# Optimization experiments

Measured on AMD Instinct MI355X. Metric: run time of the kernel, lower is better.

## Reference

```python
import jax, jax.numpy as jnp
import numpy as np

BS, N_LINKS, MAX_LEN = 8192, 512, 32
D_LINK, D_PATH, D_READ, N_OUT = 32, 128, 256, 3
BN_EPS = 1e-5


def setup_inputs() -> dict:
    key = jax.random.key(0)
    ks = jax.random.split(key, 16)
    capa = jax.random.uniform(ks[0], (BS, N_LINKS), jnp.float32, 0.5, 1.0) * 100.0
    avail = jax.random.uniform(ks[1], (BS, N_LINKS), jnp.float32) * capa
    loss = jax.random.uniform(ks[2], (BS, N_LINKS), jnp.float32) * 0.05
    demand = jax.random.uniform(ks[3], (BS,), jnp.float32) * 10.0
    path = jax.random.randint(ks[4], (BS, MAX_LEN), 0, N_LINKS)
    hop_num = jax.random.randint(ks[5], (BS,), 1, MAX_LEN + 1)
    s = 0.1
    inp = {
        "demand": demand,
        "link_avail_capacity": avail,
        "link_capacity": capa,
        "link_loss": loss,
        "path": path,
        "hop_num": hop_num,
        # GRU params (PyTorch layout: [3H, D] gates ordered r,z,n)
        "gru_w_ih": jax.random.normal(ks[6], (3 * D_PATH, D_LINK), jnp.float32) * s,
        "gru_w_hh": jax.random.normal(ks[7], (3 * D_PATH, D_PATH), jnp.float32) * s,
        "gru_b_ih": jax.random.normal(ks[8], (3 * D_PATH,), jnp.float32) * s,
        "gru_b_hh": jax.random.normal(ks[9], (3 * D_PATH,), jnp.float32) * s,
        "bn_gamma": jnp.ones((D_PATH,), jnp.float32),
        "bn_beta": jnp.zeros((D_PATH,), jnp.float32),
        # stacked readout heads [N_OUT, ...]
        "rW1": jax.random.normal(ks[10], (N_OUT, D_PATH, D_READ), jnp.float32) * s,
        "rb1": jnp.zeros((N_OUT, D_READ), jnp.float32),
        "rW2": jax.random.normal(ks[11], (N_OUT, D_READ, D_READ), jnp.float32) * s,
        "rb2": jnp.zeros((N_OUT, D_READ), jnp.float32),
        "rW3": jax.random.normal(ks[12], (N_OUT, D_READ, 1), jnp.float32) * s,
        "rb3": jnp.zeros((N_OUT, 1), jnp.float32),
    }
    return inp


def _gru_scan(x_bt, h0, w_ih, w_hh, b_ih, b_hh):
    # x_bt: [B, T, D]; h0: [B, H] -> outputs [B, T, H]
    H = h0.shape[-1]
    def step(h, x_t):
        gi = x_t @ w_ih.T + b_ih          # [B, 3H]
        gh = h @ w_hh.T + b_hh            # [B, 3H]
        i_r, i_z, i_n = gi[:, :H], gi[:, H:2*H], gi[:, 2*H:]
        h_r, h_z, h_n = gh[:, :H], gh[:, H:2*H], gh[:, 2*H:]
        r = jax.nn.sigmoid(i_r + h_r)
        z = jax.nn.sigmoid(i_z + h_z)
        n = jnp.tanh(i_n + r * h_n)
        h_new = (1.0 - z) * n + z * h
        return h_new, h_new
    _, outs = jax.lax.scan(step, h0, jnp.swapaxes(x_bt, 0, 1))
    return jnp.swapaxes(outs, 0, 1)


def reference(demand, link_avail_capacity, link_capacity, link_loss, path, hop_num,
              gru_w_ih, gru_w_hh, gru_b_ih, gru_b_hh, bn_gamma, bn_beta,
              rW1, rb1, rW2, rb2, rW3, rb3):
    bs, n_links = link_capacity.shape
    max_len = path.shape[1]
    max_capa = jax.lax.stop_gradient(jnp.max(link_capacity))
    # link_state: [B, n_links, D_LINK]; first D_LINK-4 channels are zeros
    feats = jnp.stack([
        link_avail_capacity / max_capa,
        link_capacity / max_capa,
        link_avail_capacity / link_capacity,
        link_loss,
    ], axis=-1)
    link_state = jnp.concatenate(
        [jnp.zeros((bs, n_links, D_LINK - 4), feats.dtype), feats], axis=-1)
    link_state = jax.lax.stop_gradient(link_state)  # original detaches
    # initial hidden: zeros except last channel = demand/max_capa
    h0 = jnp.concatenate(
        [jnp.zeros((bs, D_PATH - 1), feats.dtype), (demand / max_capa)[:, None]], axis=-1)
    # fused gather of link states along each path, masked past hop_num
    gathered = jnp.take_along_axis(link_state, path[:, :, None], axis=1)  # [B, T, D]
    mask = (jnp.arange(max_len)[None, :] < hop_num[:, None])[:, :, None]
    link_inputs = gathered * mask.astype(gathered.dtype)
    outputs = _gru_scan(link_inputs, h0, gru_w_ih, gru_w_hh, gru_b_ih, gru_b_hh)
    # extract hidden state at last hop of each path
    idx = (hop_num - 1)[:, None, None]
    flow = jnp.take_along_axis(outputs, idx, axis=1)[:, 0, :]  # [B, H]
    # BatchNorm1d (training mode: batch statistics, biased variance)
    mean = jnp.mean(flow, axis=0)
    var = jnp.mean((flow - mean) ** 2, axis=0)
    flow = (flow - mean) * jax.lax.rsqrt(var + BN_EPS) * bn_gamma + bn_beta
    # readout heads: Linear -> SELU -> Linear -> SELU -> Linear
    h1 = jax.nn.selu(jnp.einsum('bh,uhr->ubr', flow, rW1) + rb1[:, None, :])
    h2 = jax.nn.selu(jnp.einsum('ubr,urs->ubs', h1, rW2) + rb2[:, None, :])
    y = jnp.einsum('ubs,uso->ubo', h2, rW3) + rb3[:, None, :]  # [U, B, 1]
    return jnp.transpose(y[:, :, 0], (1, 0))  # [B, U]
```

## Files before the change

kernel.cpp:

```cpp
#include <hip/hip_runtime.h>


#define BS 8192
#define NL 512
#define ML 32
#define DP 128
#define DR 256
#define NJOB 512
#define ST 172

#define OFF_SUM    64
#define OFF_SSQ    192
#define OFF_CUR    576
#define OFF_PERM   640
#define OFF_WHH16  (OFF_PERM + BS)
#define OFF_W1     (OFF_WHH16 + 24576)
#define OFF_W2     (OFF_W1 + 49152)
#define OFF_FEATS  (OFF_W2 + 98304)
#define OFF_FLOW   (OFF_FEATS + BS*ML*4)

#define MAX_BLOCKS   256
#define WPREP_BLOCKS 336
#define SORT_BID     (MAX_BLOCKS + WPREP_BLOCKS)
#define PREP_GRID    (SORT_BID + 1)

#define KS (-1.44269504088896340736f)
#define KT ( 2.88539008177792681472f)

typedef _Float16 f16x8 __attribute__((ext_vector_type(8)));
typedef _Float16 f16x4 __attribute__((ext_vector_type(4)));
typedef float    f32x4 __attribute__((ext_vector_type(4)));

__device__ __forceinline__ float sig2_(float x){
  return __builtin_amdgcn_rcpf(1.0f + exp2f(x));
}
__device__ __forceinline__ float tanh2_(float v){
  return fmaf(-2.0f, __builtin_amdgcn_rcpf(1.0f + exp2f(v)), 1.0f);
}
__device__ __forceinline__ float seluf_(float x){
  const float sc = 1.0507009873554805f, al = 1.6732632423543772f;
  return x > 0.0f ? sc*x : sc*al*(__expf(x)-1.0f);
}

__global__ void prep_all(const int* __restrict__ path, const int* __restrict__ hop,
                         const float* __restrict__ avail, const float* __restrict__ capa,
                         const float* __restrict__ loss, const float* __restrict__ whh,
                         const float* __restrict__ rW1, const float* __restrict__ rW2,
                         float* ws){
  const int bid = blockIdx.x;
  const int tid = threadIdx.x;

  if (bid < MAX_BLOCKS){
    const float4* c4 = (const float4*)capa;
    const int n4 = BS*NL/4;
    float m = 0.0f;
    for (int i = bid*256 + tid; i < n4; i += MAX_BLOCKS*256){
      float4 v = c4[i];
      m = fmaxf(m, fmaxf(fmaxf(v.x, v.y), fmaxf(v.z, v.w)));
    }
    #pragma unroll
    for (int o = 32; o > 0; o >>= 1) m = fmaxf(m, __shfl_down(m, o, 64));
    if ((tid & 63) == 0) atomicMax((int*)ws, __float_as_int(m));
  } else if (bid < SORT_BID){
    _Float16* whh16 = (_Float16*)(ws + OFF_WHH16);
    _Float16* w1    = (_Float16*)(ws + OFF_W1);
    _Float16* w2    = (_Float16*)(ws + OFF_W2);
    int base = (bid - MAX_BLOCKS)*1024 + tid*4;
    if (base < 49152){
      const float s = (base < 32768) ? KS : KT;
      const float4 v = *(const float4*)(whh + base);
      f16x4 o = { (_Float16)(v.x*s), (_Float16)(v.y*s),
                  (_Float16)(v.z*s), (_Float16)(v.w*s) };
      *(f16x4*)(whh16 + base) = o;
    } else if (base < 147456){
      int j = base - 49152; int u = j >> 15; int rem = j & 32767; int n = rem >> 7; int k = rem & 127;
      const float* src = rW1 + u*32768 + k*256 + n;
      f16x4 o = { (_Float16)src[0], (_Float16)src[256], (_Float16)src[512], (_Float16)src[768] };
      *(f16x4*)(w1 + j) = o;
    } else {
      int j = base - 147456; int u = j >> 16; int rem = j & 65535; int n = rem >> 8; int k = rem & 255;
      const float* src = rW2 + u*65536 + k*256 + n;
      f16x4 o = { (_Float16)src[0], (_Float16)src[256], (_Float16)src[512], (_Float16)src[768] };
      *(f16x4*)(w2 + j) = o;
    }
  } else {
    __shared__ int hist[32], start[32];
    for (int i = 64 + tid; i < 640; i += 256) ws[i] = 0.0f;
    if (tid < 32) hist[tid] = 0;
    __syncthreads();
    for (int b = tid; b < BS; b += 256) atomicAdd(&hist[32 - hop[b]], 1);
    __syncthreads();
    if (tid == 0){ int acc = 0; for (int i = 0; i < 32; ++i){ start[i] = acc; acc += hist[i]; } }
    __syncthreads();
    int* perm = (int*)ws + OFF_PERM;
    for (int b = tid; b < BS; b += 256){
      int pos = atomicAdd(&start[32 - hop[b]], 1);
      perm[pos] = b;
    }
  }
}

__launch_bounds__(512, 4)
__global__ void kgru(const float* __restrict__ demand, const int* __restrict__ hop,
                     const float* __restrict__ wih, const float* __restrict__ bih,
                     const float* __restrict__ bhh,
                     const float* __restrict__ avail, const float* __restrict__ capa,
                     const float* __restrict__ loss, const int* __restrict__ path,
                     float* __restrict__ ws, float* __restrict__ flow){
  __shared__ _Float16 hA[2][16*ST];
  const int tid  = threadIdx.x;
  const int w    = tid >> 6;
  const int lane = tid & 63;
  const int lm   = lane & 15;
  const int qd   = lane >> 4;
  const int ch   = w*16 + lm;
  const float inv_maxc = 1.0f / ws[0];
  const int* perm = (const int*)ws + OFF_PERM;
  const _Float16* whh16 = (const _Float16*)(ws + OFF_WHH16);

  const int bid = blockIdx.x;
  const int q = (bid < 256) ? bid : 767 - bid;

  for (int idx = tid; idx < 1024; idx += 512){
    const int buf = idx >> 9;
    const int rem = idx & 511;
    const int m   = rem >> 5;
    const int c   = 128 + (rem & 31);
    hA[buf][m*ST + c] = (_Float16)0.f;
  }

  f16x8 bfr[5], bfz[5], bfnh[4], bfni;
  #pragma unroll
  for (int kc = 0; kc < 4; ++kc){
    bfr[kc]  = *(const f16x8*)(whh16 + (      ch)*128 + kc*32 + qd*8);
    bfz[kc]  = *(const f16x8*)(whh16 + (128 + ch)*128 + kc*32 + qd*8);
    bfnh[kc] = *(const f16x8*)(whh16 + (256 + ch)*128 + kc*32 + qd*8);
  }
  bfr[4] = (f16x8)0; bfz[4] = (f16x8)0; bfni = (f16x8)0;
  if (qd == 0){
    #pragma unroll
    for (int j = 0; j < 4; ++j){
      float s = (j < 2) ? inv_maxc : 1.0f;
      bfr[4][j] = (_Float16)(wih[(      ch)*32 + 28 + j] * s * KS);
      bfz[4][j] = (_Float16)(wih[(128 + ch)*32 + 28 + j] * s * KS);
      bfni[j]   = (_Float16)(wih[(256 + ch)*32 + 28 + j] * s * KT);
    }
  }
  const float bR  = (bih[ch]     + bhh[ch]    ) * KS;
  const float bZ  = (bih[128+ch] + bhh[128+ch]) * KS;
  const float bNI = bih[256+ch] * KT;
  const float bNH = bhh[256+ch] * KT;

  int it[4], hp[4];
  #pragma unroll
  for (int r = 0; r < 4; ++r){
    it[r] = perm[q*16 + qd*4 + r];
    hp[r] = hop[it[r]];
  }
  int tmax = max(max(hp[0],hp[1]), max(hp[2],hp[3]));
  tmax = max(tmax, __shfl_xor(tmax, 16, 64));
  tmax = max(tmax, __shfl_xor(tmax, 32, 64));

  const int  fw_i = w*2 + (lane >> 2);
  const int  fw_c = lane & 3;
  const bool fw   = (lane < 8);
  const float* pX   = avail;
  const int*   pPath = path;
  if (fw){
    const int fw_b = perm[q*16 + fw_i];
    pX = ((fw_c == 0) ? avail : (fw_c == 3) ? loss : capa) + fw_b*NL;
    pPath = path + fw_b*ML;
  }

  __syncthreads();

  float hprev[4];
  #pragma unroll
  for (int r = 0; r < 4; ++r){
    float h0 = (ch == 127) ? demand[it[r]] * inv_maxc : 0.0f;
    hprev[r] = h0;
    hA[0][(qd*4 + r)*ST + ch] = (_Float16)h0;
  }
  float rawB = 0.f;
  int   lA   = 0;
  if (fw){
    int l0 = pPath[0];
    float r0 = pX[l0];
    float a  = __shfl(r0, lane & ~3, 64);
    float cc = __shfl(r0, (lane & ~3) | 1, 64);
    float v0 = (fw_c == 2) ? (a / cc) : r0;
    hA[0][fw_i*ST + 128 + fw_c] = (_Float16)v0;
    rawB = pX[pPath[1]];
    lA   = pPath[2];
  }
  __syncthreads();

  for (int t = 0; t < tmax; ++t){
    const int cur = t & 1, nxt = cur ^ 1;

    float rawN = 0.f; int lN = 0;
    if (fw){
      rawN = pX[lA];
      int t3 = t + 3; t3 = (t3 < ML) ? t3 : (ML - 1);
      lN = pPath[t3];
      float a  = __shfl(rawB, lane & ~3, 64);
      float cc = __shfl(rawB, (lane & ~3) | 1, 64);
      float v  = (fw_c == 2) ? (a / cc) : rawB;
      hA[nxt][fw_i*ST + 128 + fw_c] = (_Float16)v;
    }

    f32x4 accr  = {bR, bR, bR, bR};
    f32x4 accz  = {bZ, bZ, bZ, bZ};
    f32x4 accnh = {bNH, bNH, bNH, bNH};
    f32x4 accni = {bNI, bNI, bNI, bNI};
    #pragma unroll
    for (int kc = 0; kc < 5; ++kc){
      f16x8 a = *(const f16x8*)(&hA[cur][lm*ST + kc*32 + qd*8]);
      accr = __builtin_amdgcn_mfma_f32_16x16x32_f16(a, bfr[kc], accr, 0, 0, 0);
      accz = __builtin_amdgcn_mfma_f32_16x16x32_f16(a, bfz[kc], accz, 0, 0, 0);
      if (kc < 4)
        accnh = __builtin_amdgcn_mfma_f32_16x16x32_f16(a, bfnh[kc], accnh, 0, 0, 0);
      else
        accni = __builtin_amdgcn_mfma_f32_16x16x32_f16(a, bfni, accni, 0, 0, 0);
    }

    #pragma unroll
    for (int r = 0; r < 4; ++r){
      float rr = sig2_(accr[r]);
      float zz = sig2_(accz[r]);
      float nn = tanh2_(fmaf(rr, accnh[r], accni[r]));
      float hn = fmaf(zz, hprev[r] - nn, nn);
      if (t < hp[r]) hprev[r] = hn;
      hA[nxt][(qd*4 + r)*ST + ch] = (_Float16)hprev[r];
    }
    rawB = rawN; lA = lN;
    __syncthreads();
  }

  float ssum = 0.f, ssq = 0.f;
  #pragma unroll
  for (int r = 0; r < 4; ++r){
    float v = hprev[r];
    flow[it[r]*DP + ch] = v;
    ssum += v;
    ssq  = fmaf(v, v, ssq);
  }
  ssum += __shfl_xor(ssum, 16, 64);  ssum += __shfl_xor(ssum, 32, 64);
  ssq  += __shfl_xor(ssq,  16, 64);  ssq  += __shfl_xor(ssq,  32, 64);
  if (qd == 0){
    atomicAdd(&ws[OFF_SUM + ch], ssum);
    atomicAdd(&ws[OFF_SSQ + ch], ssq);
  }
}

__launch_bounds__(256, 4)
__global__ void kmlp(const float* __restrict__ flow, const float* __restrict__ ws,
                     const float* __restrict__ gamma, const float* __restrict__ beta,
                     const float* __restrict__ rb1, const float* __restrict__ rb2,
                     const float* __restrict__ rW3, const float* __restrict__ rb3,
                     float* __restrict__ out){
  __shared__ _Float16 x_lds[32*136];
  __shared__ _Float16 h1_lds[32*264];
  __shared__ float aa[DP], bb[DP];
  __shared__ float y_part[4][32];
  const int tid  = threadIdx.x;
  const int w    = tid >> 6;
  const int lane = tid & 63;
  const int lm   = lane & 15;
  const int qd   = lane >> 4;
  const int b0   = blockIdx.x * 32;
  const int u    = blockIdx.y;
  const _Float16* w1 = (const _Float16*)(ws + OFF_W1) + u*(DR*DP);
  const _Float16* w2 = (const _Float16*)(ws + OFF_W2) + u*(DR*DR);

  if (tid < DP){
    float m = ws[OFF_SUM + tid] * (1.0f/BS);
    float q = ws[OFF_SSQ + tid] * (1.0f/BS);
    float rstd = rsqrtf(q - m*m + 1e-5f);
    float a = rstd * gamma[tid];
    aa[tid] = a;
    bb[tid] = fmaf(-m, a, beta[tid]);
  }
  __syncthreads();

  for (int idx = tid; idx < 32*DP; idx += 256){
    int i = idx >> 7, h = idx & 127;
    x_lds[i*136 + h] = (_Float16)fmaf(flow[(b0 + i)*DP + h], aa[h], bb[h]);
  }
  __syncthreads();

  for (int nt = 0; nt < 4; ++nt){
    const int n = (4*w + nt)*16 + lm;
    const float bias1 = rb1[u*DR + n];
    f16x8 b1[4];
    #pragma unroll
    for (int kc = 0; kc < 4; ++kc)
      b1[kc] = *(const f16x8*)(w1 + n*DP + kc*32 + qd*8);
    #pragma unroll
    for (int mt = 0; mt < 2; ++mt){
      f32x4 acc = {bias1, bias1, bias1, bias1};
      #pragma unroll
      for (int kc = 0; kc < 4; ++kc){
        f16x8 a1 = *(const f16x8*)(&x_lds[(mt*16 + lm)*136 + kc*32 + qd*8]);
        acc = __builtin_amdgcn_mfma_f32_16x16x32_f16(a1, b1[kc], acc, 0, 0, 0);
      }
      #pragma unroll
      for (int r = 0; r < 4; ++r)
        h1_lds[(mt*16 + qd*4 + r)*264 + n] = (_Float16)seluf_(acc[r]);
    }
  }
  __syncthreads();

  {
    float p[2][4] = {{0.f,0.f,0.f,0.f},{0.f,0.f,0.f,0.f}};
    for (int nt = 0; nt < 4; ++nt){
      const int n = (4*w + nt)*16 + lm;
      const float bias2 = rb2[u*DR + n];
      const float w3l   = rW3[u*DR + n];
      f16x8 b2[8];
      #pragma unroll
      for (int kc = 0; kc < 8; ++kc)
        b2[kc] = *(const f16x8*)(w2 + n*DR + kc*32 + qd*8);
      #pragma unroll
      for (int mt = 0; mt < 2; ++mt){
        f32x4 acc = {bias2, bias2, bias2, bias2};
        #pragma unroll
        for (int kc = 0; kc < 8; ++kc){
          f16x8 a2 = *(const f16x8*)(&h1_lds[(mt*16 + lm)*264 + kc*32 + qd*8]);
          acc = __builtin_amdgcn_mfma_f32_16x16x32_f16(a2, b2[kc], acc, 0, 0, 0);
        }
        #pragma unroll
        for (int r = 0; r < 4; ++r)
          p[mt][r] += seluf_(acc[r]) * w3l;
      }
    }
    #pragma unroll
    for (int mt = 0; mt < 2; ++mt){
      #pragma unroll
      for (int r = 0; r < 4; ++r){
        float v = p[mt][r];
        v += __shfl_xor(v, 1, 64);
        v += __shfl_xor(v, 2, 64);
        v += __shfl_xor(v, 4, 64);
        v += __shfl_xor(v, 8, 64);
        if (lm == 0) y_part[w][mt*16 + qd*4 + r] = v;
      }
    }
  }
  __syncthreads();
  if (tid < 32){
    float y = y_part[0][tid] + y_part[1][tid] + y_part[2][tid] + y_part[3][tid] + rb3[u];
    out[(b0 + tid)*3 + u] = y;
  }
}

extern "C" void kernel_launch(void* const* d_in, const int* in_sizes, int n_in,
                              void* d_out, int out_size, void* d_ws, size_t ws_size,
                              hipStream_t stream){
  const float* demand = (const float*)d_in[0];
  const float* avail  = (const float*)d_in[1];
  const float* capa   = (const float*)d_in[2];
  const float* loss   = (const float*)d_in[3];
  const int*   path   = (const int*)d_in[4];
  const int*   hop    = (const int*)d_in[5];
  const float* wih    = (const float*)d_in[6];
  const float* whh    = (const float*)d_in[7];
  const float* bih    = (const float*)d_in[8];
  const float* bhh    = (const float*)d_in[9];
  const float* gamma  = (const float*)d_in[10];
  const float* beta   = (const float*)d_in[11];
  const float* rW1    = (const float*)d_in[12];
  const float* rb1    = (const float*)d_in[13];
  const float* rW2    = (const float*)d_in[14];
  const float* rb2    = (const float*)d_in[15];
  const float* rW3    = (const float*)d_in[16];
  const float* rb3    = (const float*)d_in[17];
  float* ws  = (float*)d_ws;
  float* out = (float*)d_out;

  prep_all <<<PREP_GRID, 256, 0, stream>>>(path, hop, avail, capa, loss,
                                           whh, rW1, rW2, ws);
  kgru     <<<NJOB, 512, 0, stream>>>(demand, hop, wih, bih, bhh,
                                      avail, capa, loss, path, ws, ws + OFF_FLOW);
  kmlp     <<<dim3(BS/32, 3), 256, 0, stream>>>(ws + OFF_FLOW, ws, gamma, beta,
                                                rb1, rb2, rW3, rb3, out);
}
```

Before: 207.0 us.

## Preload path link features into LDS and shrink input MFMA to 16x16x16

Before the recurrence, each GRU block gathers all per-step link features for its 16 paths into a shared-memory buffer. This replaces the per-step global loads and prefetch pipeline done by a few lanes. The input contribution now uses a smaller 16x16x16 MFMA reading from that buffer, and the hidden-state LDS tile stride shrinks. The W_hh fp16 conversion moves out of the prep kernel into kgru's register load. The cost is about 20KB of extra LDS per block, which may reduce occupancy, plus redundant whh conversion in every block.

```diff
diff --git a/kernel.cpp b/kernel.cpp
--- a/kernel.cpp
+++ b/kernel.cpp
@@ -7,7 +7,7 @@
 #define DP 128
 #define DR 256
 #define NJOB 512
-#define ST 172
+#define ST 140
 
 #define OFF_SUM    64
 #define OFF_SSQ    192
@@ -20,7 +20,7 @@
 #define OFF_FLOW   (OFF_FEATS + BS*ML*4)
 
 #define MAX_BLOCKS   256
-#define WPREP_BLOCKS 336
+#define WPREP_BLOCKS 288
 #define SORT_BID     (MAX_BLOCKS + WPREP_BLOCKS)
 #define PREP_GRID    (SORT_BID + 1)
 
@@ -62,23 +62,16 @@
     for (int o = 32; o > 0; o >>= 1) m = fmaxf(m, __shfl_down(m, o, 64));
     if ((tid & 63) == 0) atomicMax((int*)ws, __float_as_int(m));
   } else if (bid < SORT_BID){
-    _Float16* whh16 = (_Float16*)(ws + OFF_WHH16);
-    _Float16* w1    = (_Float16*)(ws + OFF_W1);
-    _Float16* w2    = (_Float16*)(ws + OFF_W2);
+    _Float16* w1 = (_Float16*)(ws + OFF_W1);
+    _Float16* w2 = (_Float16*)(ws + OFF_W2);
     int base = (bid - MAX_BLOCKS)*1024 + tid*4;
-    if (base < 49152){
-      const float s = (base < 32768) ? KS : KT;
-      const float4 v = *(const float4*)(whh + base);
-      f16x4 o = { (_Float16)(v.x*s), (_Float16)(v.y*s),
-                  (_Float16)(v.z*s), (_Float16)(v.w*s) };
-      *(f16x4*)(whh16 + base) = o;
-    } else if (base < 147456){
-      int j = base - 49152; int u = j >> 15; int rem = j & 32767; int n = rem >> 7; int k = rem & 127;
+    if (base < 98304){
+      int j = base; int u = j >> 15; int rem = j & 32767; int n = rem >> 7; int k = rem & 127;
       const float* src = rW1 + u*32768 + k*256 + n;
       f16x4 o = { (_Float16)src[0], (_Float16)src[256], (_Float16)src[512], (_Float16)src[768] };
       *(f16x4*)(w1 + j) = o;
     } else {
-      int j = base - 147456; int u = j >> 16; int rem = j & 65535; int n = rem >> 8; int k = rem & 255;
+      int j = base - 98304; int u = j >> 16; int rem = j & 65535; int n = rem >> 8; int k = rem & 255;
       const float* src = rW2 + u*65536 + k*256 + n;
       f16x4 o = { (_Float16)src[0], (_Float16)src[256], (_Float16)src[512], (_Float16)src[768] };
       *(f16x4*)(w2 + j) = o;
@@ -102,12 +95,14 @@
 
 __launch_bounds__(512, 4)
 __global__ void kgru(const float* __restrict__ demand, const int* __restrict__ hop,
-                     const float* __restrict__ wih, const float* __restrict__ bih,
-                     const float* __restrict__ bhh,
+                     const float* __restrict__ wih, const float* __restrict__ whh,
+                     const float* __restrict__ bih, const float* __restrict__ bhh,
                      const float* __restrict__ avail, const float* __restrict__ capa,
                      const float* __restrict__ loss, const int* __restrict__ path,
                      float* __restrict__ ws, float* __restrict__ flow){
   __shared__ _Float16 hA[2][16*ST];
+  __shared__ __align__(16) _Float16 feats16[32*320];
+  __shared__ int bl_it[16], bl_hp[16];
   const int tid  = threadIdx.x;
   const int w    = tid >> 6;
   const int lane = tid & 63;
@@ -116,34 +111,37 @@
   const int ch   = w*16 + lm;
   const float inv_maxc = 1.0f / ws[0];
   const int* perm = (const int*)ws + OFF_PERM;
-  const _Float16* whh16 = (const _Float16*)(ws + OFF_WHH16);
 
   const int bid = blockIdx.x;
   const int q = (bid < 256) ? bid : 767 - bid;
 
-  for (int idx = tid; idx < 1024; idx += 512){
-    const int buf = idx >> 9;
-    const int rem = idx & 511;
-    const int m   = rem >> 5;
-    const int c   = 128 + (rem & 31);
-    hA[buf][m*ST + c] = (_Float16)0.f;
-  }
-
-  f16x8 bfr[5], bfz[5], bfnh[4], bfni;
+  if (tid < 16){ int b = perm[q*16 + tid]; bl_it[tid] = b; bl_hp[tid] = hop[b]; }
+  {
+    int* fz = (int*)feats16;
+    for (int i = tid; i < 32*320/2; i += 512) fz[i] = 0;
+  }
+
+  f16x8 bfr[4], bfz[4], bfnh[4];
   #pragma unroll
   for (int kc = 0; kc < 4; ++kc){
-    bfr[kc]  = *(const f16x8*)(whh16 + (      ch)*128 + kc*32 + qd*8);
-    bfz[kc]  = *(const f16x8*)(whh16 + (128 + ch)*128 + kc*32 + qd*8);
-    bfnh[kc] = *(const f16x8*)(whh16 + (256 + ch)*128 + kc*32 + qd*8);
-  }
-  bfr[4] = (f16x8)0; bfz[4] = (f16x8)0; bfni = (f16x8)0;
+    const float* pr = whh + (      ch)*128 + kc*32 + qd*8;
+    const float* pz = whh + (128 + ch)*128 + kc*32 + qd*8;
+    const float* pn = whh + (256 + ch)*128 + kc*32 + qd*8;
+    #pragma unroll
+    for (int j = 0; j < 8; ++j){
+      bfr[kc][j]  = (_Float16)(pr[j] * KS);
+      bfz[kc][j]  = (_Float16)(pz[j] * KS);
+      bfnh[kc][j] = (_Float16)(pn[j] * KT);
+    }
+  }
+  f16x4 bfr4 = (f16x4)0, bfz4 = (f16x4)0, bfni = (f16x4)0;
   if (qd == 0){
     #pragma unroll
     for (int j = 0; j < 4; ++j){
       float s = (j < 2) ? inv_maxc : 1.0f;
-      bfr[4][j] = (_Float16)(wih[(      ch)*32 + 28 + j] * s * KS);
-      bfz[4][j] = (_Float16)(wih[(128 + ch)*32 + 28 + j] * s * KS);
-      bfni[j]   = (_Float16)(wih[(256 + ch)*32 + 28 + j] * s * KT);
+      bfr4[j] = (_Float16)(wih[(      ch)*32 + 28 + j] * s * KS);
+      bfz4[j] = (_Float16)(wih[(128 + ch)*32 + 28 + j] * s * KS);
+      bfni[j] = (_Float16)(wih[(256 + ch)*32 + 28 + j] * s * KT);
     }
   }
   const float bR  = (bih[ch]     + bhh[ch]    ) * KS;
@@ -151,28 +149,33 @@
   const float bNI = bih[256+ch] * KT;
   const float bNH = bhh[256+ch] * KT;
 
+  __syncthreads();
+
+  #pragma unroll
+  for (int jj = 0; jj < 4; ++jj){
+    int u = tid + jj*512;
+    int item = u >> 7, t = (u >> 2) & 31, c = u & 3;
+    int b = bl_it[item];
+    if (t < bl_hp[item]){
+      int l = path[b*ML + t];
+      float v;
+      if (c == 0)      v = avail[b*NL + l];
+      else if (c == 1) v = capa [b*NL + l];
+      else if (c == 3) v = loss [b*NL + l];
+      else             v = avail[b*NL + l] / capa[b*NL + l];
+      feats16[t*320 + item*20 + c] = (_Float16)v;
+    }
+  }
+
   int it[4], hp[4];
   #pragma unroll
   for (int r = 0; r < 4; ++r){
-    it[r] = perm[q*16 + qd*4 + r];
-    hp[r] = hop[it[r]];
+    it[r] = bl_it[qd*4 + r];
+    hp[r] = bl_hp[qd*4 + r];
   }
   int tmax = max(max(hp[0],hp[1]), max(hp[2],hp[3]));
   tmax = max(tmax, __shfl_xor(tmax, 16, 64));
   tmax = max(tmax, __shfl_xor(tmax, 32, 64));
-
-  const int  fw_i = w*2 + (lane >> 2);
-  const int  fw_c = lane & 3;
-  const bool fw   = (lane < 8);
-  const float* pX   = avail;
-  const int*   pPath = path;
-  if (fw){
-    const int fw_b = perm[q*16 + fw_i];
-    pX = ((fw_c == 0) ? avail : (fw_c == 3) ? loss : capa) + fw_b*NL;
-    pPath = path + fw_b*ML;
-  }
-
-  __syncthreads();
 
   float hprev[4];
   #pragma unroll
@@ -181,47 +184,27 @@
     hprev[r] = h0;
     hA[0][(qd*4 + r)*ST + ch] = (_Float16)h0;
   }
-  float rawB = 0.f;
-  int   lA   = 0;
-  if (fw){
-    int l0 = pPath[0];
-    float r0 = pX[l0];
-    float a  = __shfl(r0, lane & ~3, 64);
-    float cc = __shfl(r0, (lane & ~3) | 1, 64);
-    float v0 = (fw_c == 2) ? (a / cc) : r0;
-    hA[0][fw_i*ST + 128 + fw_c] = (_Float16)v0;
-    rawB = pX[pPath[1]];
-    lA   = pPath[2];
-  }
   __syncthreads();
 
   for (int t = 0; t < tmax; ++t){
     const int cur = t & 1, nxt = cur ^ 1;
-
-    float rawN = 0.f; int lN = 0;
-    if (fw){
-      rawN = pX[lA];
-      int t3 = t + 3; t3 = (t3 < ML) ? t3 : (ML - 1);
-      lN = pPath[t3];
-      float a  = __shfl(rawB, lane & ~3, 64);
-      float cc = __shfl(rawB, (lane & ~3) | 1, 64);
-      float v  = (fw_c == 2) ? (a / cc) : rawB;
-      hA[nxt][fw_i*ST + 128 + fw_c] = (_Float16)v;
-    }
 
     f32x4 accr  = {bR, bR, bR, bR};
     f32x4 accz  = {bZ, bZ, bZ, bZ};
     f32x4 accnh = {bNH, bNH, bNH, bNH};
     f32x4 accni = {bNI, bNI, bNI, bNI};
     #pragma unroll
-    for (int kc = 0; kc < 5; ++kc){
+    for (int kc = 0; kc < 4; ++kc){
       f16x8 a = *(const f16x8*)(&hA[cur][lm*ST + kc*32 + qd*8]);
-      accr = __builtin_amdgcn_mfma_f32_16x16x32_f16(a, bfr[kc], accr, 0, 0, 0);
-      accz = __builtin_amdgcn_mfma_f32_16x16x32_f16(a, bfz[kc], accz, 0, 0, 0);
-      if (kc < 4)
-        accnh = __builtin_amdgcn_mfma_f32_16x16x32_f16(a, bfnh[kc], accnh, 0, 0, 0);
-      else
-        accni = __builtin_amdgcn_mfma_f32_16x16x32_f16(a, bfni, accni, 0, 0, 0);
+      accr  = __builtin_amdgcn_mfma_f32_16x16x32_f16(a, bfr[kc],  accr,  0, 0, 0);
+      accz  = __builtin_amdgcn_mfma_f32_16x16x32_f16(a, bfz[kc],  accz,  0, 0, 0);
+      accnh = __builtin_amdgcn_mfma_f32_16x16x32_f16(a, bfnh[kc], accnh, 0, 0, 0);
+    }
+    {
+      f16x4 af = *(const f16x4*)(&feats16[t*320 + lm*20 + qd*4]);
+      accr = __builtin_amdgcn_mfma_f32_16x16x16f16(af, bfr4, accr, 0, 0, 0);
+      accz = __builtin_amdgcn_mfma_f32_16x16x16f16(af, bfz4, accz, 0, 0, 0);
+      accni= __builtin_amdgcn_mfma_f32_16x16x16f16(af, bfni, accni, 0, 0, 0);
     }
 
     #pragma unroll
@@ -233,7 +216,6 @@
       if (t < hp[r]) hprev[r] = hn;
       hA[nxt][(qd*4 + r)*ST + ch] = (_Float16)hprev[r];
     }
-    rawB = rawN; lA = lN;
     __syncthreads();
   }
 
@@ -380,7 +362,7 @@
 
   prep_all <<<PREP_GRID, 256, 0, stream>>>(path, hop, avail, capa, loss,
                                            whh, rW1, rW2, ws);
-  kgru     <<<NJOB, 512, 0, stream>>>(demand, hop, wih, bih, bhh,
+  kgru     <<<NJOB, 512, 0, stream>>>(demand, hop, wih, whh, bih, bhh,
                                       avail, capa, loss, path, ws, ws + OFF_FLOW);
   kmlp     <<<dim3(BS/32, 3), 256, 0, stream>>>(ws + OFF_FLOW, ws, gamma, beta,
                                                 rb1, rb2, rW3, rb3, out);
```

Result: slower. 214.8 us (+3.7%).
